# Optimization experiments

Measured on AMD Instinct MI355X. Metric: run time of the kernel, lower is better.

## Reference

```python
import jax, jax.numpy as jnp
import numpy as np
from jax import lax

B, IN_C, OUT_C, K, Z_DIM, H, W = 32, 128, 128, 3, 64, 96, 96
PAD = K // 2


def setup_inputs() -> dict:
    key = jax.random.key(0)
    k1, k2, k3, k4, k5, k6 = jax.random.split(key, 6)
    fan = (2.0 / (IN_C * K * K)) ** 0.5
    x = jax.random.normal(k1, (B, IN_C, H, W), dtype=jnp.float32)
    z = jax.random.normal(k2, (B, Z_DIM), dtype=jnp.float32)
    base_weight = jax.random.normal(k3, (OUT_C, IN_C, K, K), dtype=jnp.float32) * fan
    # torch nn.Linear weights are [out_features, in_features]
    gate_weight = jax.random.normal(k4, (OUT_C, Z_DIM), dtype=jnp.float32) * (1.0 / Z_DIM ** 0.5)
    pw_weight = jax.random.normal(k5, (OUT_C * IN_C, Z_DIM), dtype=jnp.float32) * (1.0 / Z_DIM ** 0.5)
    dw_weight = jax.random.normal(k6, (OUT_C * K * K, Z_DIM), dtype=jnp.float32) * (1.0 / Z_DIM ** 0.5)
    return {"x": x, "z": z, "base_weight": base_weight, "gate_weight": gate_weight,
            "pw_weight": pw_weight, "dw_weight": dw_weight}


def _merged_weight(z, base_weight, gate_weight, pw_weight, dw_weight):
    # BaseOp.get_weight: base * gate(z)  -> [B, out_c, in_c, k, k]
    gate = z @ gate_weight.T                       # [B, out_c]
    w_base = base_weight[None] * gate[:, :, None, None, None]
    # PWOp.get_weight (groups=1): [B, out_c, in_c, 1, 1]
    pw = (z @ pw_weight.T).reshape(B, OUT_C, IN_C)
    # DWOp.get_weight: [B, out_c, 1, k, k]
    dw = (z @ dw_weight.T).reshape(B, OUT_C, 1, K, K)
    # delta = pw * dw broadcast -> [B, out_c, in_c, k, k]
    delta = pw[:, :, :, None, None] * dw
    return w_base + delta


def _per_sample_conv(xi, wi):
    # xi: [in_c, H, W], wi: [out_c, in_c, k, k]
    return lax.conv_general_dilated(
        xi[None], wi, window_strides=(1, 1),
        padding=((PAD, PAD), (PAD, PAD)),
        dimension_numbers=("NCHW", "OIHW", "NCHW"))[0]


def reference(x, z, base_weight, gate_weight, pw_weight, dw_weight):
    w = _merged_weight(z, base_weight, gate_weight, pw_weight, dw_weight)
    return jax.vmap(_per_sample_conv)(x, w)  # [B, out_c, H, W]
```

## Files before the change

kernel.cpp:

```cpp
#include <hip/hip_runtime.h>
#include <hip/hip_bf16.h>

typedef __bf16 bf16x8 __attribute__((ext_vector_type(8)));
typedef float f32x4 __attribute__((ext_vector_type(4)));

__device__ __forceinline__ int swz(int n, int k) {
  int pair = n >> 1;
  int s = (((n & 1) << 2) | k) ^ (pair & 7);
  return (pair << 7) + (s << 4);
}

__device__ __forceinline__ void load_lds16(const void* g, void* l) {
  __builtin_amdgcn_global_load_lds((const __attribute__((address_space(1))) void*)g,
                                   (__attribute__((address_space(3))) void*)l, 16, 0, 0);
}

__global__ __launch_bounds__(512) void prep_x_kernel(const float* __restrict__ x,
                                                     __hip_bfloat16* __restrict__ xn) {
  __shared__ float tile[128][97];
  int h = blockIdx.x;
  int b = blockIdx.y;
  const float* src = x + (size_t)b * 128 * 9216 + h * 96;
  for (int f = threadIdx.x; f < 3072; f += 512) {
    int ic = f / 24, w4 = f - ic * 24;
    float4 v = *(const float4*)(src + (size_t)ic * 9216 + w4 * 4);
    tile[ic][w4 * 4 + 0] = v.x; tile[ic][w4 * 4 + 1] = v.y;
    tile[ic][w4 * 4 + 2] = v.z; tile[ic][w4 * 4 + 3] = v.w;
  }
  __syncthreads();
  __hip_bfloat16* bb  = xn + (size_t)b * 4 * 307328;
  __hip_bfloat16* dst = bb + (h + 1) * 3136 + 32;
  for (int o = threadIdx.x; o < 1536; o += 512) {
    int grp = o / 384, rem = o - grp * 384;
    int w = rem >> 2, chunk = rem & 3;
    __hip_bfloat16 tmp[8];
    #pragma unroll
    for (int e = 0; e < 8; e++) tmp[e] = __float2bfloat16(tile[grp * 32 + chunk * 8 + e][w]);
    *(uint4*)(dst + (size_t)grp * 307328 + w * 32 + chunk * 8) = *(uint4*)tmp;
  }
  if (threadIdx.x < 32) {
    int u = threadIdx.x;
    int grp = u >> 3, rem = u & 7;
    int pw = (rem >> 2) ? 97 : 0, k = rem & 3;
    *(uint4*)(bb + (size_t)grp * 307328 + ((h + 1) * 98 + pw) * 32 + k * 8) = make_uint4(0, 0, 0, 0);
  }
  if (h == 0 || h == 95) {
    int ph = (h == 0) ? 0 : 97;
    for (int u = threadIdx.x; u < 1568; u += 512) {
      int grp = u / 392, rem = u - grp * 392;
      int pw = rem >> 2, k = rem & 3;
      *(uint4*)(bb + (size_t)grp * 307328 + (ph * 98 + pw) * 32 + k * 8) = make_uint4(0, 0, 0, 0);
    }
  }
}

__global__ __launch_bounds__(256) void prep_w_kernel(
    const float* __restrict__ z, const float* __restrict__ gw,
    const float* __restrict__ pww, const float* __restrict__ dww,
    const float* __restrict__ base, __hip_bfloat16* __restrict__ Wt) {
  __shared__ float zs[2048];
  __shared__ float res[138][33];
  int oc = blockIdx.x;
  for (int i = threadIdx.x; i < 2048; i += 256) zs[i] = z[i];
  __syncthreads();
  int row = threadIdx.x;
  if (row < 138) {
    const float* wrow = (row == 0) ? gw + (size_t)oc * 64
                      : (row < 10) ? dww + ((size_t)oc * 9 + (row - 1)) * 64
                                   : pww + ((size_t)oc * 128 + (row - 10)) * 64;
    float wr[64];
    #pragma unroll
    for (int i = 0; i < 16; i++) {
      float4 v = ((const float4*)wrow)[i];
      wr[4*i] = v.x; wr[4*i+1] = v.y; wr[4*i+2] = v.z; wr[4*i+3] = v.w;
    }
    for (int b = 0; b < 32; b++) {
      float a = 0.f;
      #pragma unroll
      for (int i = 0; i < 64; i++) a += zs[b * 64 + i] * wr[i];
      res[row][b] = a;
    }
  }
  __syncthreads();
  for (int e = threadIdx.x; e < 18432; e += 256) {
    int icp = e & 15;
    int r1 = e >> 4;
    int tap = r1 % 9, bg = r1 / 9;
    int grp = bg & 3, b = bg >> 2;
    int ic = grp * 32 + icp * 2;
    float g = res[0][b], d = res[1 + tap][b];
    float p0 = res[10 + ic][b], p1 = res[11 + ic][b];
    const float* bp = base + ((size_t)(oc * 128 + ic)) * 9 + tap;
    __hip_bfloat162 o2 = {__float2bfloat16(bp[0] * g + p0 * d),
                          __float2bfloat16(bp[9] * g + p1 * d)};
    *(__hip_bfloat162*)(Wt + (((size_t)bg * 9 + tap) * 128 + oc) * 32 + icp * 2) = o2;
  }
}

__global__ __launch_bounds__(256, 3) void conv_kernel(
    const __hip_bfloat16* __restrict__ xn, const __hip_bfloat16* __restrict__ Wt,
    float* __restrict__ out) {
  __shared__ __align__(16) char smem[49152];
  char* const xt  = smem;
  char* const wb0 = smem + 24576;
  char* const wb1 = smem + 36864;

  int bid = blockIdx.x;
  int X = bid & 7, q = bid >> 3;
  int logical = X * 288 + q;
  int b   = logical / 72;
  int rem = logical - b * 72;
  int ocg = rem & 1;
  int t36 = rem >> 1;
  int hr  = t36 / 3;
  int wc  = t36 - hr * 3;
  int h0 = hr * 8, w0 = wc * 32;

  int tid = threadIdx.x;
  int lane = tid & 63, wid = tid >> 6;
  int l15 = lane & 15, lk = lane >> 4;

  int xoff[6];
  #pragma unroll
  for (int j = 0; j < 6; j++) {
    int p = j * 256 + tid; if (p > 1359) p = 1359;
    int pair = p >> 3, v = (p & 7) ^ (pair & 7);
    int n = (pair << 1) | (v >> 2), k = v & 3;
    int hh = n / 34, ww = n - hh * 34;
    xoff[j] = ((h0 + hh) * 98 + (w0 + ww)) * 32 + k * 8;
  }
  int wsoff[3];
  #pragma unroll
  for (int i = 0; i < 3; i++) {
    int p = i * 256 + tid;
    int pair = p >> 3, v = (p & 7) ^ (pair & 7);
    int n = (pair << 1) | (v >> 2), k = v & 3;
    int dx = n >> 6, ocl = n & 63;
    wsoff[i] = (dx * 128 + ocg * 64 + ocl) * 32 + k * 8;
  }

  const __hip_bfloat16* xbase = xn + (size_t)b * 4 * 307328;
  const __hip_bfloat16* wbase = Wt + (size_t)b * 147456;

  f32x4 acc[4][4];
  #pragma unroll
  for (int i = 0; i < 4; i++)
    #pragma unroll
    for (int j = 0; j < 4; j++) acc[i][j] = (f32x4){0.f, 0.f, 0.f, 0.f};

  #pragma unroll
  for (int i = 0; i < 3; i++)
    load_lds16(wbase + wsoff[i], wb0 + ((i * 256 + wid * 64) << 4));
  #pragma unroll
  for (int j = 0; j < 6; j++)
    load_lds16(xbase + xoff[j], xt + ((j * 256 + wid * 64) << 4));

#define PHASE(G, T, WCUR, WNXT, DOX, DOW, VM)                                      \
  {                                                                                \
    __builtin_amdgcn_s_barrier();                                                  \
    if (DOX) {                                                                     \
      const __hip_bfloat16* xsrc = xbase + (size_t)(G) * 307328;                   \
      _Pragma("unroll")                                                            \
      for (int j = 0; j < 6; j++)                                                  \
        load_lds16(xsrc + xoff[j], xt + ((j * 256 + wid * 64) << 4));              \
    }                                                                              \
    if (DOW) {                                                                     \
      const __hip_bfloat16* wsrc = wbase + (size_t)((G) * 9 + (T) * 3 + 3) * 4096; \
      _Pragma("unroll")                                                            \
      for (int i = 0; i < 3; i++)                                                  \
        load_lds16(wsrc + wsoff[i], (WNXT) + ((i * 256 + wid * 64) << 4));         \
    }                                                                              \
    asm volatile("s_waitcnt vmcnt(" #VM ")" ::: "memory");                         \
    __builtin_amdgcn_s_barrier();                                                  \
    _Pragma("unroll")                                                              \
    for (int dx = 0; dx < 3; dx++) {                                               \
      bf16x8 bfr[4], afr[4];                                                       \
      _Pragma("unroll")                                                            \
      for (int j = 0; j < 4; j++)                                                  \
        bfr[j] = *(const bf16x8*)((WCUR) + swz(dx * 64 + j * 16 + l15, lk));       \
      _Pragma("unroll")                                                            \
      for (int i = 0; i < 4; i++) {                                                \
        int r = wid * 2 + (i >> 1) + (T);                                          \
        int c = ((i & 1) << 4) + l15 + dx;                                         \
        afr[i] = *(const bf16x8*)(xt + swz(r * 34 + c, lk));                       \
      }                                                                            \
      __builtin_amdgcn_s_setprio(1);                                               \
      _Pragma("unroll")                                                            \
      for (int i = 0; i < 4; i++)                                                  \
        _Pragma("unroll")                                                          \
        for (int j = 0; j < 4; j++)                                                \
          acc[i][j] = __builtin_amdgcn_mfma_f32_16x16x32_bf16(afr[i], bfr[j],      \
                                                              acc[i][j], 0, 0, 0); \
      __builtin_amdgcn_s_setprio(0);                                               \
    }                                                                              \
  }

  PHASE(0, 0, wb0, wb1, 0, 1, 3)
  PHASE(0, 1, wb1, wb0, 0, 1, 3)
  PHASE(0, 2, wb0, wb1, 0, 1, 3)
  PHASE(1, 0, wb1, wb0, 1, 1, 3)
  PHASE(1, 1, wb0, wb1, 0, 1, 3)
  PHASE(1, 2, wb1, wb0, 0, 1, 3)
  PHASE(2, 0, wb0, wb1, 1, 1, 3)
  PHASE(2, 1, wb1, wb0, 0, 1, 3)
  PHASE(2, 2, wb0, wb1, 0, 1, 3)
  PHASE(3, 0, wb1, wb0, 1, 1, 3)
  PHASE(3, 1, wb0, wb1, 0, 1, 3)
  PHASE(3, 2, wb1, wb0, 0, 0, 0)
#undef PHASE

  float* ob = out + ((size_t)b * 128 + ocg * 64) * 9216;
  #pragma unroll
  for (int j = 0; j < 4; j++) {
    int oc = j * 16 + l15;
    float* op = ob + (size_t)oc * 9216 + h0 * 96 + w0 + lk * 4;
    #pragma unroll
    for (int i = 0; i < 4; i++) {
      int m0 = wid * 64 + i * 16;
      *(f32x4*)(op + (m0 >> 5) * 96 + (m0 & 31)) = acc[i][j];
    }
  }
}

extern "C" void kernel_launch(void* const* d_in, const int* in_sizes, int n_in,
                              void* d_out, int out_size, void* d_ws, size_t ws_size,
                              hipStream_t stream) {
  const float* x   = (const float*)d_in[0];
  const float* z   = (const float*)d_in[1];
  const float* bw  = (const float*)d_in[2];
  const float* gw  = (const float*)d_in[3];
  const float* pww = (const float*)d_in[4];
  const float* dww = (const float*)d_in[5];
  float* out = (float*)d_out;

  char* ws = (char*)d_ws;
  __hip_bfloat16* xn = (__hip_bfloat16*)ws;
  __hip_bfloat16* Wt = (__hip_bfloat16*)(ws + 78675968);

  hipLaunchKernelGGL(prep_x_kernel, dim3(96, 32), dim3(512), 0, stream, x, xn);
  hipLaunchKernelGGL(prep_w_kernel, dim3(128), dim3(256), 0, stream,
                     z, gw, pww, dww, bw, Wt);
  hipLaunchKernelGGL(conv_kernel,   dim3(2304), dim3(256), 0, stream, xn, Wt, out);
}
```

Baseline: 161.6 us.

## Retile conv to 6x32x128 blocks with 32x32 MFMA and 4-deep weight ring

Each block now computes all 128 output channels for a 6-row by 32-column spatial tile, instead of 64 channels over 8x32. This drops the two-way output-channel split, so each input tile is loaded once instead of twice. The inner loop switches from 16x16x32 to 32x32x16 bf16 MFMA over 36 per-tap phases. Weights stream through a 4-slot LDS ring with a prefetch distance of two taps, and the input tile is reloaded only when the channel group changes. The trade-off is a larger 2x2 wave layout and more accumulator registers, plus more barriers per block (one per tap instead of one per tap-row).

```diff
diff --git a/kernel.cpp b/kernel.cpp
--- a/kernel.cpp
+++ b/kernel.cpp
@@ -3,6 +3,7 @@
 
 typedef __bf16 bf16x8 __attribute__((ext_vector_type(8)));
 typedef float f32x4 __attribute__((ext_vector_type(4)));
+typedef float f32x16 __attribute__((ext_vector_type(16)));
 
 __device__ __forceinline__ int swz(int n, int k) {
   int pair = n >> 1;
@@ -100,124 +101,144 @@
 __global__ __launch_bounds__(256, 3) void conv_kernel(
     const __hip_bfloat16* __restrict__ xn, const __hip_bfloat16* __restrict__ Wt,
     float* __restrict__ out) {
-  __shared__ __align__(16) char smem[49152];
-  char* const xt  = smem;
-  char* const wb0 = smem + 24576;
-  char* const wb1 = smem + 36864;
+  __shared__ __align__(16) char smem[50176];
+  char* const wqb = smem;
+  char* const xt  = smem + 32768;
 
   int bid = blockIdx.x;
   int X = bid & 7, q = bid >> 3;
-  int logical = X * 288 + q;
-  int b   = logical / 72;
-  int rem = logical - b * 72;
-  int ocg = rem & 1;
-  int t36 = rem >> 1;
-  int hr  = t36 / 3;
-  int wc  = t36 - hr * 3;
-  int h0 = hr * 8, w0 = wc * 32;
+  int logical = X * 192 + q;
+  int b   = logical / 48;
+  int rem = logical - b * 48;
+  int hr  = rem / 3;
+  int wc  = rem - hr * 3;
+  int h0 = hr * 6, w0 = wc * 32;
 
   int tid = threadIdx.x;
   int lane = tid & 63, wid = tid >> 6;
-  int l15 = lane & 15, lk = lane >> 4;
-
-  int xoff[6];
-  #pragma unroll
-  for (int j = 0; j < 6; j++) {
-    int p = j * 256 + tid; if (p > 1359) p = 1359;
+  int l31 = lane & 31, lh = lane >> 5;
+  int wm = wid >> 1, wn = wid & 1;
+
+  int ar[3];
+  #pragma unroll
+  for (int i = 0; i < 3; i++) ar[i] = (wm * 3 + i) * 34 + l31;
+  int boff[2][2];
+  #pragma unroll
+  for (int j = 0; j < 2; j++)
+    #pragma unroll
+    for (int kk = 0; kk < 2; kk++)
+      boff[j][kk] = swz(wn * 64 + j * 32 + l31, kk * 2 + lh);
+
+  int xoff[5];
+  #pragma unroll
+  for (int j = 0; j < 5; j++) {
+    int p = (j < 4) ? (j * 256 + tid) : (1024 + lane);
     int pair = p >> 3, v = (p & 7) ^ (pair & 7);
     int n = (pair << 1) | (v >> 2), k = v & 3;
     int hh = n / 34, ww = n - hh * 34;
     xoff[j] = ((h0 + hh) * 98 + (w0 + ww)) * 32 + k * 8;
   }
-  int wsoff[3];
-  #pragma unroll
-  for (int i = 0; i < 3; i++) {
+  int woff[2];
+  #pragma unroll
+  for (int i = 0; i < 2; i++) {
     int p = i * 256 + tid;
     int pair = p >> 3, v = (p & 7) ^ (pair & 7);
     int n = (pair << 1) | (v >> 2), k = v & 3;
-    int dx = n >> 6, ocl = n & 63;
-    wsoff[i] = (dx * 128 + ocg * 64 + ocl) * 32 + k * 8;
+    woff[i] = n * 32 + k * 8;
   }
 
   const __hip_bfloat16* xbase = xn + (size_t)b * 4 * 307328;
   const __hip_bfloat16* wbase = Wt + (size_t)b * 147456;
 
-  f32x4 acc[4][4];
-  #pragma unroll
-  for (int i = 0; i < 4; i++)
-    #pragma unroll
-    for (int j = 0; j < 4; j++) acc[i][j] = (f32x4){0.f, 0.f, 0.f, 0.f};
-
+  f32x16 acc[3][2];
   #pragma unroll
   for (int i = 0; i < 3; i++)
-    load_lds16(wbase + wsoff[i], wb0 + ((i * 256 + wid * 64) << 4));
-  #pragma unroll
-  for (int j = 0; j < 6; j++)
+    #pragma unroll
+    for (int j = 0; j < 2; j++)
+      #pragma unroll
+      for (int e = 0; e < 16; e++) acc[i][j][e] = 0.f;
+
+  #pragma unroll
+  for (int i = 0; i < 2; i++)
+    load_lds16(wbase + woff[i], wqb + ((i * 256 + wid * 64) << 4));
+  #pragma unroll
+  for (int i = 0; i < 2; i++)
+    load_lds16(wbase + 4096 + woff[i], wqb + 8192 + ((i * 256 + wid * 64) << 4));
+  #pragma unroll
+  for (int j = 0; j < 4; j++)
     load_lds16(xbase + xoff[j], xt + ((j * 256 + wid * 64) << 4));
-
-#define PHASE(G, T, WCUR, WNXT, DOX, DOW, VM)                                      \
+  load_lds16(xbase + xoff[4], xt + (1024 << 4));
+
+#define PH(S, VM, XBAR)                                                            \
   {                                                                                \
-    __builtin_amdgcn_s_barrier();                                                  \
-    if (DOX) {                                                                     \
-      const __hip_bfloat16* xsrc = xbase + (size_t)(G) * 307328;                   \
-      _Pragma("unroll")                                                            \
-      for (int j = 0; j < 6; j++)                                                  \
+    constexpr int grp_ = (S) / 9, tap_ = (S) % 9;                                  \
+    constexpr int dy_ = tap_ / 3, dx_ = tap_ % 3;                                  \
+    if (XBAR) {                                                                    \
+      __builtin_amdgcn_s_barrier();                                                \
+      const __hip_bfloat16* xsrc = xbase + (size_t)grp_ * 307328;                  \
+      _Pragma("unroll")                                                            \
+      for (int j = 0; j < 4; j++)                                                  \
         load_lds16(xsrc + xoff[j], xt + ((j * 256 + wid * 64) << 4));              \
+      load_lds16(xsrc + xoff[4], xt + (1024 << 4));                                \
     }                                                                              \
-    if (DOW) {                                                                     \
-      const __hip_bfloat16* wsrc = wbase + (size_t)((G) * 9 + (T) * 3 + 3) * 4096; \
-      _Pragma("unroll")                                                            \
-      for (int i = 0; i < 3; i++)                                                  \
-        load_lds16(wsrc + wsoff[i], (WNXT) + ((i * 256 + wid * 64) << 4));         \
+    if ((S) + 2 <= 35) {                                                           \
+      const __hip_bfloat16* wsrc = wbase + (size_t)((S) + 2) * 4096;               \
+      _Pragma("unroll")                                                            \
+      for (int i = 0; i < 2; i++)                                                  \
+        load_lds16(wsrc + woff[i],                                                 \
+                   wqb + ((((S) + 2) & 3) << 13) + ((i * 256 + wid * 64) << 4));   \
     }                                                                              \
     asm volatile("s_waitcnt vmcnt(" #VM ")" ::: "memory");                         \
     __builtin_amdgcn_s_barrier();                                                  \
+    const char* wc_ = wqb + (((S) & 3) << 13);                                     \
+    bf16x8 bfr[2][2], afr[3][2];                                                   \
     _Pragma("unroll")                                                              \
-    for (int dx = 0; dx < 3; dx++) {                                               \
-      bf16x8 bfr[4], afr[4];                                                       \
-      _Pragma("unroll")                                                            \
-      for (int j = 0; j < 4; j++)                                                  \
-        bfr[j] = *(const bf16x8*)((WCUR) + swz(dx * 64 + j * 16 + l15, lk));       \
-      _Pragma("unroll")                                                            \
-      for (int i = 0; i < 4; i++) {                                                \
-        int r = wid * 2 + (i >> 1) + (T);                                          \
-        int c = ((i & 1) << 4) + l15 + dx;                                         \
-        afr[i] = *(const bf16x8*)(xt + swz(r * 34 + c, lk));                       \
-      }                                                                            \
-      __builtin_amdgcn_s_setprio(1);                                               \
-      _Pragma("unroll")                                                            \
-      for (int i = 0; i < 4; i++)                                                  \
+    for (int j = 0; j < 2; j++)                                                    \
+      _Pragma("unroll")                                                            \
+      for (int kk = 0; kk < 2; kk++)                                               \
+        bfr[j][kk] = *(const bf16x8*)(wc_ + boff[j][kk]);                          \
+    _Pragma("unroll")                                                              \
+    for (int i = 0; i < 3; i++) {                                                  \
+      int n_ = ar[i] + (dy_ * 34 + dx_);                                           \
+      _Pragma("unroll")                                                            \
+      for (int kk = 0; kk < 2; kk++)                                               \
+        afr[i][kk] = *(const bf16x8*)(xt + swz(n_, kk * 2 + lh));                  \
+    }                                                                              \
+    __builtin_amdgcn_s_setprio(1);                                                 \
+    _Pragma("unroll")                                                              \
+    for (int i = 0; i < 3; i++)                                                    \
+      _Pragma("unroll")                                                            \
+      for (int j = 0; j < 2; j++)                                                  \
         _Pragma("unroll")                                                          \
-        for (int j = 0; j < 4; j++)                                                \
-          acc[i][j] = __builtin_amdgcn_mfma_f32_16x16x32_bf16(afr[i], bfr[j],      \
-                                                              acc[i][j], 0, 0, 0); \
-      __builtin_amdgcn_s_setprio(0);                                               \
-    }                                                                              \
-  }
-
-  PHASE(0, 0, wb0, wb1, 0, 1, 3)
-  PHASE(0, 1, wb1, wb0, 0, 1, 3)
-  PHASE(0, 2, wb0, wb1, 0, 1, 3)
-  PHASE(1, 0, wb1, wb0, 1, 1, 3)
-  PHASE(1, 1, wb0, wb1, 0, 1, 3)
-  PHASE(1, 2, wb1, wb0, 0, 1, 3)
-  PHASE(2, 0, wb0, wb1, 1, 1, 3)
-  PHASE(2, 1, wb1, wb0, 0, 1, 3)
-  PHASE(2, 2, wb0, wb1, 0, 1, 3)
-  PHASE(3, 0, wb1, wb0, 1, 1, 3)
-  PHASE(3, 1, wb0, wb1, 0, 1, 3)
-  PHASE(3, 2, wb1, wb0, 0, 0, 0)
-#undef PHASE
-
-  float* ob = out + ((size_t)b * 128 + ocg * 64) * 9216;
-  #pragma unroll
-  for (int j = 0; j < 4; j++) {
-    int oc = j * 16 + l15;
-    float* op = ob + (size_t)oc * 9216 + h0 * 96 + w0 + lk * 4;
-    #pragma unroll
-    for (int i = 0; i < 4; i++) {
-      int m0 = wid * 64 + i * 16;
-      *(f32x4*)(op + (m0 >> 5) * 96 + (m0 & 31)) = acc[i][j];
+        for (int kk = 0; kk < 2; kk++)                                             \
+          acc[i][j] = __builtin_amdgcn_mfma_f32_32x32x16_bf16(afr[i][kk],          \
+                          bfr[j][kk], acc[i][j], 0, 0, 0);                         \
+    __builtin_amdgcn_s_setprio(0);                                                 \
+  }
+
+  PH(0, 2, 0)  PH(1, 4, 0)  PH(2, 4, 0)  PH(3, 4, 0)  PH(4, 4, 0)  PH(5, 4, 0)
+  PH(6, 4, 0)  PH(7, 4, 0)  PH(8, 4, 0)
+  PH(9, 2, 1)  PH(10, 4, 0) PH(11, 4, 0) PH(12, 4, 0) PH(13, 4, 0) PH(14, 4, 0)
+  PH(15, 4, 0) PH(16, 4, 0) PH(17, 4, 0)
+  PH(18, 2, 1) PH(19, 4, 0) PH(20, 4, 0) PH(21, 4, 0) PH(22, 4, 0) PH(23, 4, 0)
+  PH(24, 4, 0) PH(25, 4, 0) PH(26, 4, 0)
+  PH(27, 2, 1) PH(28, 4, 0) PH(29, 4, 0) PH(30, 4, 0) PH(31, 4, 0) PH(32, 4, 0)
+  PH(33, 4, 0) PH(34, 2, 0) PH(35, 0, 0)
+#undef PH
+
+  #pragma unroll
+  for (int i = 0; i < 3; i++) {
+    int h = h0 + wm * 3 + i;
+    #pragma unroll
+    for (int j = 0; j < 2; j++) {
+      int oc = wn * 64 + j * 32 + l31;
+      float* op = out + ((size_t)b * 128 + oc) * 9216 + h * 96 + w0 + 4 * lh;
+      #pragma unroll
+      for (int qq = 0; qq < 4; qq++) {
+        f32x4 v = {acc[i][j][4 * qq + 0], acc[i][j][4 * qq + 1],
+                   acc[i][j][4 * qq + 2], acc[i][j][4 * qq + 3]};
+        *(f32x4*)(op + 8 * qq) = v;
+      }
     }
   }
 }
@@ -240,5 +261,5 @@
   hipLaunchKernelGGL(prep_x_kernel, dim3(96, 32), dim3(512), 0, stream, x, xn);
   hipLaunchKernelGGL(prep_w_kernel, dim3(128), dim3(256), 0, stream,
                      z, gw, pww, dww, bw, Wt);
-  hipLaunchKernelGGL(conv_kernel,   dim3(2304), dim3(256), 0, stream, xn, Wt, out);
-}
+  hipLaunchKernelGGL(conv_kernel,   dim3(1536), dim3(256), 0, stream, xn, Wt, out);
+}
```

Result: slower. 204.3 us (+26.4%).
